# Kernel tuning notes

Measured on AMD Instinct MI355X. Metric: run time of the kernel, lower is better.

## Reference

```python
import jax, jax.numpy as jnp
import numpy as np
import math

NUM_SOLU, BS, GS, ED, NH = 10, 32, 1000, 128, 8
KD = ED // NH
MSH = 16
NEG = -9e15


def setup_inputs() -> dict:
    key = jax.random.key(0)
    ks = jax.random.split(key, 16)
    node_embed = jax.random.normal(ks[0], (BS, GS, ED), jnp.float32)
    # random TSP tours: permutations per (solution, batch) -> each node a source exactly once
    solutions = jnp.argsort(jax.random.uniform(ks[1], (NUM_SOLU, BS, GS)), axis=-1).astype(jnp.int32)
    costs = jax.random.uniform(ks[2], (NUM_SOLU, BS), minval=1.0, maxval=2.0)  # positive tour costs
    dist = jax.random.uniform(ks[3], (BS, GS, GS), jnp.float32)
    solution_embed_old = jax.random.normal(ks[4], (BS, GS, ED), jnp.float32)
    s = 1.0 / math.sqrt(ED)
    Wq = jax.random.uniform(ks[5], (ED, ED), minval=-s, maxval=s)
    Wk = jax.random.uniform(ks[6], (ED, ED), minval=-s, maxval=s)
    m1 = math.sqrt(0.5)
    m2 = math.sqrt(1.0 / 16.0)
    mix1_weight = jax.random.uniform(ks[7], (NH, 2, MSH), minval=-m1, maxval=m1)
    mix1_bias = jax.random.uniform(ks[8], (NH, MSH), minval=-m1, maxval=m1)
    mix2_weight = jax.random.uniform(ks[9], (NH, MSH, 1), minval=-m2, maxval=m2)
    mix2_bias = jax.random.uniform(ks[10], (NH, 1), minval=-m2, maxval=m2)
    sh = 1.0 / math.sqrt(NH)
    norm_head_w = jax.random.uniform(ks[11], (NH,), minval=-sh, maxval=sh)
    sg = 1.0 / math.sqrt(ED)
    gru_w_ih = jax.random.uniform(ks[12], (3 * ED, ED), minval=-sg, maxval=sg)
    gru_w_hh = jax.random.uniform(ks[13], (3 * ED, ED), minval=-sg, maxval=sg)
    gru_b_ih = jax.random.uniform(ks[14], (3 * ED,), minval=-sg, maxval=sg)
    gru_b_hh = jax.random.uniform(ks[15], (3 * ED,), minval=-sg, maxval=sg)
    return dict(node_embed=node_embed, solutions=solutions, costs=costs, dist=dist,
                solution_embed_old=solution_embed_old, Wq=Wq, Wk=Wk,
                mix1_weight=mix1_weight, mix1_bias=mix1_bias,
                mix2_weight=mix2_weight, mix2_bias=mix2_bias,
                norm_head_w=norm_head_w, gru_w_ih=gru_w_ih, gru_w_hh=gru_w_hh,
                gru_b_ih=gru_b_ih, gru_b_hh=gru_b_hh)


def _forward(node_embed, costs, dist, solution_embed_old, Wq, Wk,
             mix1_weight, mix1_bias, mix2_weight, mix2_bias, norm_head_w,
             gru_w_ih, gru_w_hh, gru_b_ih, gru_b_hh, solutions):
    norm_factor = 1.0 / math.sqrt(KD)
    sqrt_qkv = KD ** 0.5
    nxt = jnp.roll(solutions, -1, axis=-1)                      # [S,B,T] successor in tour
    b_idx = jnp.arange(BS)[None, :, None]
    emb_solu = node_embed[b_idx, solutions]                     # [S,B,T,E] gather
    emb_next = node_embed[b_idx, nxt]                           # [S,B,T,E]
    q = (emb_solu @ Wq.T).reshape(NUM_SOLU, BS, GS, NH, KD)
    k = (emb_next @ Wk.T).reshape(NUM_SOLU, BS, GS, NH, KD)
    dot = jnp.einsum('sbthd,sbthd->sbth', q, k) * (norm_factor / sqrt_qkv)
    edge_cost = dist[b_idx, solutions, nxt]                     # [S,B,T]
    two = jnp.stack([dot, jnp.broadcast_to(edge_cost[..., None], dot.shape)], -1)  # [S,B,T,H,2]
    ms1 = jax.nn.relu(jnp.einsum('sbthe,hem->sbthm', two, mix1_weight) + mix1_bias)
    ms2 = jnp.einsum('sbthm,hmo->sbtho', ms1, mix2_weight)[..., 0] + mix2_bias[:, 0]  # [S,B,T,H]
    e = jnp.einsum('sbth,h->sbt', ms2, norm_head_w)             # norm_head Linear(n_heads,1)
    cost = e / costs[:, :, None]                                # [S,B,T]
    # scatter-add edge scores into dense [B,G,G] attention (tours = permutations,
    # so each (b, src) appears once per solution -> add == per-solution set + sum)
    bb = jnp.broadcast_to(b_idx, solutions.shape)
    attn = jnp.zeros((BS, GS, GS), node_embed.dtype).at[
        bb.reshape(-1), solutions.reshape(-1), nxt.reshape(-1)].add(cost.reshape(-1))
    attn = jnp.where(attn != 0.0, attn, NEG)
    ar = jnp.arange(GS)
    attn = attn.at[:, ar, ar].set(NEG)
    attn = jax.nn.softmax(attn, axis=-1)
    solu_embed = attn @ node_embed                              # [B,G,E]
    # torch GRUCell: gates order r,z,n
    x = solu_embed.reshape(-1, ED)
    h = solution_embed_old.reshape(-1, ED)
    gi = x @ gru_w_ih.T + gru_b_ih
    gh = h @ gru_w_hh.T + gru_b_hh
    i_r, i_z, i_n = jnp.split(gi, 3, axis=-1)
    h_r, h_z, h_n = jnp.split(gh, 3, axis=-1)
    r = jax.nn.sigmoid(i_r + h_r)
    z = jax.nn.sigmoid(i_z + h_z)
    n = jnp.tanh(i_n + r * h_n)
    new = ((1.0 - z) * n + z * h).reshape(BS, GS, ED)
    return jnp.stack([jax.nn.elu(new), new])                    # [2,B,G,E]


def reference(node_embed, solutions, costs, dist, solution_embed_old, Wq, Wk,
              mix1_weight, mix1_bias, mix2_weight, mix2_bias, norm_head_w,
              gru_w_ih, gru_w_hh, gru_b_ih, gru_b_hh):
    out = _forward(node_embed, costs, dist, solution_embed_old, Wq, Wk,
                   mix1_weight, mix1_bias, mix2_weight, mix2_bias, norm_head_w,
                   gru_w_ih, gru_w_hh, gru_b_ih, gru_b_hh, solutions)
    return (out[0], out[1])
```

## Files before the change

### kernel.cpp

```cpp
#include <hip/hip_runtime.h>
#include <math.h>

#define NS 10
#define NB 32
#define NG 1000
#define NE 128
#define NH 8
#define MSH 16

typedef __bf16 bf16x8 __attribute__((ext_vector_type(8)));
typedef float f32x4 __attribute__((ext_vector_type(4)));
typedef unsigned short ushort;
typedef ushort us8 __attribute__((ext_vector_type(8)));

__device__ __forceinline__ ushort f2bf(float f) {
    union { float f; unsigned u; } c; c.f = f;
    unsigned r = c.u + 0x7FFFu + ((c.u >> 16) & 1u);
    return (ushort)(r >> 16);
}
__device__ __forceinline__ float bflo(unsigned u) {
    union { unsigned v; float f; } c; c.v = u << 16; return c.f;
}
__device__ __forceinline__ float bfhi(unsigned u) {
    union { unsigned v; float f; } c; c.v = u & 0xFFFF0000u; return c.f;
}
__device__ __forceinline__ float dot8(uint4 q, uint4 k) {
    return bflo(q.x) * bflo(k.x) + bfhi(q.x) * bfhi(k.x)
         + bflo(q.y) * bflo(k.y) + bfhi(q.y) * bfhi(k.y)
         + bflo(q.z) * bflo(k.z) + bfhi(q.z) * bfhi(k.z)
         + bflo(q.w) * bflo(k.w) + bfhi(q.w) * bfhi(k.w);
}

__global__ __launch_bounds__(512) void qk_prep(
        const float* __restrict__ ne,
        const int* __restrict__ sol, const float* __restrict__ dist,
        const float* __restrict__ Wq, const float* __restrict__ Wk,
        const float* __restrict__ wih, const float* __restrict__ whh,
        ushort* __restrict__ QKb, ushort* __restrict__ ne_b,
        int* __restrict__ succ, float* __restrict__ edge_val,
        ushort* __restrict__ wih_b, ushort* __restrict__ whh_b) {
    const int tid = threadIdx.x;
    if (blockIdx.x >= 500) {
        const int bid2 = blockIdx.x - 500;
        if (bid2 < 625) {
            const int gidx = bid2 * 512 + tid;
            const int sb = gidx / NG;
            const int t = gidx - sb * NG;
            const int* srow = sol + (size_t)sb * NG;
            const int src = srow[t];
            const int tn = (t + 1 == NG) ? 0 : t + 1;
            const int dst = srow[tn];
            const int b = sb & 31;
            succ[(size_t)sb * NG + src] = dst;
            edge_val[(size_t)sb * NG + src] = dist[(size_t)(b * NG + src) * NG + dst];
        } else {
            const int wt = (bid2 - 625) * 512 + tid;
            const int e = wt * 8;
            const float* src = (e < 49152) ? wih : whh;
            ushort* dst = (e < 49152) ? wih_b : whh_b;
            const int off = (e < 49152) ? e : e - 49152;
            const float4 f0 = ((const float4*)(src + off))[0];
            const float4 f1 = ((const float4*)(src + off))[1];
            us8 v;
            v[0] = f2bf(f0.x); v[1] = f2bf(f0.y); v[2] = f2bf(f0.z); v[3] = f2bf(f0.w);
            v[4] = f2bf(f1.x); v[5] = f2bf(f1.y); v[6] = f2bf(f1.z); v[7] = f2bf(f1.w);
            *(us8*)(dst + off) = v;
        }
        return;
    }

    __shared__ __align__(16) ushort A[64 * 128];
    const int rowbase = blockIdx.x * 64;
    {
#pragma unroll
        for (int i2 = 0; i2 < 2; ++i2) {
            const int i = tid + i2 * 512;
            const int r = i >> 4, kc = i & 15;
            const float4* s4 = (const float4*)(ne + (size_t)(rowbase + r) * NE);
            const float4 f0 = s4[kc * 2], f1 = s4[kc * 2 + 1];
            us8 v;
            v[0] = f2bf(f0.x); v[1] = f2bf(f0.y); v[2] = f2bf(f0.z); v[3] = f2bf(f0.w);
            v[4] = f2bf(f1.x); v[5] = f2bf(f1.y); v[6] = f2bf(f1.z); v[7] = f2bf(f1.w);
            *(us8*)&A[(r * 16 + (kc ^ (r & 7))) * 8] = v;
            *(us8*)&ne_b[(size_t)(rowbase + r) * NE + kc * 8] = v;
        }
    }
    __syncthreads();

    const int w = tid >> 6, l = tid & 63;
    const int lr = l & 15, lg = l >> 4;

    f32x4 acc[4][2] = {};
#pragma unroll
    for (int ks = 0; ks < 4; ++ks) {
        bf16x8 a[4], b[2];
#pragma unroll
        for (int mf = 0; mf < 4; ++mf) {
            const int r = mf * 16 + lr;
            a[mf] = *(const bf16x8*)&A[(r * 16 + ((ks * 4 + lg) ^ (r & 7))) * 8];
        }
#pragma unroll
        for (int nf = 0; nf < 2; ++nf) {
            const int j = w * 32 + nf * 16 + lr;
            const float* Wrow = (j < 128) ? (Wq + (size_t)j * 128 + ks * 32 + lg * 8)
                                          : (Wk + (size_t)(j - 128) * 128 + ks * 32 + lg * 8);
            const float4 wf0 = ((const float4*)Wrow)[0];
            const float4 wf1 = ((const float4*)Wrow)[1];
            union { us8 u; bf16x8 bv; } cv;
            cv.u[0] = f2bf(wf0.x); cv.u[1] = f2bf(wf0.y); cv.u[2] = f2bf(wf0.z); cv.u[3] = f2bf(wf0.w);
            cv.u[4] = f2bf(wf1.x); cv.u[5] = f2bf(wf1.y); cv.u[6] = f2bf(wf1.z); cv.u[7] = f2bf(wf1.w);
            b[nf] = cv.bv;
        }
#pragma unroll
        for (int mf = 0; mf < 4; ++mf)
#pragma unroll
            for (int nf = 0; nf < 2; ++nf)
                acc[mf][nf] = __builtin_amdgcn_mfma_f32_16x16x32_bf16(a[mf], b[nf], acc[mf][nf], 0, 0, 0);
    }
#pragma unroll
    for (int mf = 0; mf < 4; ++mf)
#pragma unroll
        for (int nf = 0; nf < 2; ++nf)
#pragma unroll
            for (int q = 0; q < 4; ++q) {
                const int row = rowbase + mf * 16 + lg * 4 + q;
                const int col = w * 32 + nf * 16 + lr;
                QKb[(size_t)row * 256 + col] = f2bf(acc[mf][nf][q]);
            }
}

__global__ __launch_bounds__(256) void score_agg(
        const int* __restrict__ succ, const float* __restrict__ costs,
        const float* __restrict__ edge_val, const ushort* __restrict__ QKb,
        const ushort* __restrict__ ne_b,
        const float* __restrict__ m1w, const float* __restrict__ m1b,
        const float* __restrict__ m2w, const float* __restrict__ m2b,
        const float* __restrict__ nhw,
        unsigned* __restrict__ solu_b) {
    __shared__ float w1t[2][MSH][NH];
    __shared__ float b1t[MSH][NH];
    __shared__ float w2t[MSH][NH];
    __shared__ float b2s[NH];
    __shared__ float nws[NH];
    const int tid = threadIdx.x;
    {
        const int h = tid >> 5, e = (tid >> 4) & 1, m = tid & 15;
        w1t[e][m][h] = m1w[tid];
        if (tid < 128) {
            const int h2 = tid >> 4, m2 = tid & 15;
            b1t[m2][h2] = m1b[tid];
            w2t[m2][h2] = m2w[tid];
        }
        if (tid < NH) { b2s[tid] = m2b[tid]; nws[tid] = nhw[tid]; }
    }
    __syncthreads();

    const int bid = blockIdx.x;
    const int xcd = bid & 7;
    const int idx = bid >> 3;
    const int b = xcd + 8 * (idx / 125);
    const int gbase = (idx % 125) * 8 + ((tid >> 6) << 1);
    const int lane = tid & 63;
    const int h = lane & 7;
    const int sg = lane >> 3;

    int dstp[2][2]; float edgep[2][2];
#pragma unroll
    for (int r = 0; r < 2; ++r) {
        const size_t o0 = (size_t)(sg * NB + b) * NG + (gbase + r);
        const size_t o1 = (size_t)((8 + sg) * NB + b) * NG + (gbase + r);
        dstp[r][0] = succ[o0];
        dstp[r][1] = (sg < 2) ? succ[o1] : 0;
        edgep[r][0] = edge_val[o0];
        edgep[r][1] = (sg < 2) ? edge_val[o1] : 0.f;
    }

    uint4 kk[2][2][2];
#pragma unroll
    for (int r = 0; r < 2; ++r)
#pragma unroll
        for (int p = 0; p < 2; ++p) {
            const uint4* Kr = (const uint4*)(QKb + (size_t)(b * NG + dstp[r][p]) * 256 + 128);
            kk[r][p][0] = Kr[h * 2]; kk[r][p][1] = Kr[h * 2 + 1];
        }

    uint4 qq[2][2];
#pragma unroll
    for (int r = 0; r < 2; ++r) {
        const uint4* Qr = (const uint4*)(QKb + (size_t)(b * NG + gbase + r) * 256);
        qq[r][0] = Qr[h * 2]; qq[r][1] = Qr[h * 2 + 1];
    }

    unsigned urow[2][NS];
#pragma unroll
    for (int r = 0; r < 2; ++r) {
        int dd;
#pragma unroll
        for (int s = 0; s < 8; ++s) {
            dd = __shfl(dstp[r][0], s * 8);
            urow[r][s] = ((const unsigned*)(ne_b + (size_t)(b * NG + dd) * NE))[lane];
        }
        dd = __shfl(dstp[r][1], 0);
        urow[r][8] = ((const unsigned*)(ne_b + (size_t)(b * NG + dd) * NE))[lane];
        dd = __shfl(dstp[r][1], 8);
        urow[r][9] = ((const unsigned*)(ne_b + (size_t)(b * NG + dd) * NE))[lane];
    }

    float val_p[2][2];
#pragma unroll
    for (int r = 0; r < 2; ++r)
#pragma unroll
        for (int p = 0; p < 2; ++p) {
            float dd = (dot8(qq[r][0], kk[r][p][0]) + dot8(qq[r][1], kk[r][p][1])) * 0.0625f;
            float ms2 = b2s[h];
#pragma unroll
            for (int m = 0; m < MSH; ++m) {
                float t = fmaf(dd, w1t[0][m][h], fmaf(edgep[r][p], w1t[1][m][h], b1t[m][h]));
                t = fmaxf(t, 0.f);
                ms2 = fmaf(t, w2t[m][h], ms2);
            }
            float contrib = ms2 * nws[h];
            contrib += __shfl_xor(contrib, 1);
            contrib += __shfl_xor(contrib, 2);
            contrib += __shfl_xor(contrib, 4);
            val_p[r][p] = contrib;
        }

    const float cinv = __builtin_amdgcn_rcpf(costs[((lane < NS) ? lane : 0) * NB + b]);
#pragma unroll
    for (int r = 0; r < 2; ++r) {
        const float va = __shfl(val_p[r][0], (lane & 7) * 8);
        const float vb = __shfl(val_p[r][1], (lane & 1) * 8);
        const int   da = __shfl(dstp[r][0], (lane & 7) * 8);
        const int   db = __shfl(dstp[r][1], (lane & 1) * 8);
        float v_own = ((lane < 8) ? va : vb) * cinv;
        const int d_own = (lane < 8) ? da : db;

        float acc = v_own;
        bool first = true;
#pragma unroll
        for (int p = 0; p < NS; ++p) {
            const int   d_p = __shfl(d_own, p);
            const float v_p = __shfl(v_own, p);
            const bool eq = (d_p == d_own);
            first = first && (!eq || p >= lane);
            acc += (eq && p > lane) ? v_p : 0.f;
        }
        const bool surv = (lane < NS) && first && (acc != 0.f);

        float mval = surv ? acc : -3.0e38f;
        mval = fmaxf(mval, __shfl_xor(mval, 1));
        mval = fmaxf(mval, __shfl_xor(mval, 2));
        mval = fmaxf(mval, __shfl_xor(mval, 4));
        mval = fmaxf(mval, __shfl_xor(mval, 8));
        const float e = surv ? __expf(acc - mval) : 0.f;
        float den = e;
        den += __shfl_xor(den, 1);
        den += __shfl_xor(den, 2);
        den += __shfl_xor(den, 4);
        den += __shfl_xor(den, 8);
        const float wt_own = e * __builtin_amdgcn_rcpf(den);

        const bool any = (__ballot(surv) != 0ull);

        float a0 = 0.f, a1 = 0.f;
        if (!any) {
            const unsigned* base = (const unsigned*)(ne_b + (size_t)b * NG * NE);
            for (int n = 0; n < NG; ++n) {
                const unsigned u = base[n * 64 + lane];
                a0 += bflo(u); a1 += bfhi(u);
            }
            const float invG = 1.f / NG;
            a0 *= invG; a1 *= invG;
        } else {
#pragma unroll
            for (int s = 0; s < NS; ++s) {
                const float wt = __shfl(wt_own, s);
                a0 += wt * bflo(urow[r][s]);
                a1 += wt * bfhi(urow[r][s]);
            }
        }
        solu_b[(size_t)(b * NG + gbase + r) * 64 + lane] =
            (unsigned)f2bf(a0) | ((unsigned)f2bf(a1) << 16);
    }
}

__global__ __launch_bounds__(512) void gru_mfma(
        const ushort* __restrict__ x_b,
        const float* __restrict__ h_in,
        const ushort* __restrict__ wih_b, const ushort* __restrict__ whh_b,
        const float* __restrict__ bih, const float* __restrict__ bhh,
        float* __restrict__ out0, float* __restrict__ out1) {
    __shared__ __align__(16) ushort X[32 * 128];
    __shared__ __align__(16) ushort H[32 * 128];
    const int tid = threadIdx.x;
    const int rowbase = blockIdx.x * 32;

    {
        const int r = tid >> 4, kc = tid & 15;
        us8 xv = *(const us8*)&x_b[(size_t)(rowbase + r) * NE + kc * 8];
        *(us8*)&X[(r * 16 + (kc ^ (r & 7))) * 8] = xv;
        const float4* h4 = (const float4*)(h_in + (size_t)(rowbase + r) * NE);
        const float4 f0 = h4[kc * 2], f1 = h4[kc * 2 + 1];
        us8 hv;
        hv[0] = f2bf(f0.x); hv[1] = f2bf(f0.y); hv[2] = f2bf(f0.z); hv[3] = f2bf(f0.w);
        hv[4] = f2bf(f1.x); hv[5] = f2bf(f1.y); hv[6] = f2bf(f1.z); hv[7] = f2bf(f1.w);
        *(us8*)&H[(r * 16 + (kc ^ (r & 7))) * 8] = hv;
    }
    __syncthreads();

    const int w = tid >> 6, l = tid & 63;
    const int lr = l & 15, lg = l >> 4;
    const int j = w * 16 + lr;

    f32x4 acc[2][6] = {};
#pragma unroll
    for (int ks = 0; ks < 4; ++ks) {
        bf16x8 ax[2], ah[2], bb[6];
#pragma unroll
        for (int mf = 0; mf < 2; ++mf) {
            const int r = mf * 16 + lr;
            const int c = (r * 16 + ((ks * 4 + lg) ^ (r & 7))) * 8;
            ax[mf] = *(const bf16x8*)&X[c];
            ah[mf] = *(const bf16x8*)&H[c];
        }
#pragma unroll
        for (int g = 0; g < 3; ++g) {
            bb[g]     = *(const bf16x8*)&wih_b[(size_t)(g * 128 + j) * 128 + ks * 32 + lg * 8];
            bb[g + 3] = *(const bf16x8*)&whh_b[(size_t)(g * 128 + j) * 128 + ks * 32 + lg * 8];
        }
#pragma unroll
        for (int mf = 0; mf < 2; ++mf) {
#pragma unroll
            for (int g = 0; g < 3; ++g) {
                acc[mf][g]     = __builtin_amdgcn_mfma_f32_16x16x32_bf16(ax[mf], bb[g],     acc[mf][g],     0, 0, 0);
                acc[mf][g + 3] = __builtin_amdgcn_mfma_f32_16x16x32_bf16(ah[mf], bb[g + 3], acc[mf][g + 3], 0, 0, 0);
            }
        }
    }

    const float bi0 = bih[j], bi1 = bih[128 + j], bi2 = bih[256 + j];
    const float bh0 = bhh[j], bh1 = bhh[128 + j], bh2 = bhh[256 + j];
#pragma unroll
    for (int mf = 0; mf < 2; ++mf) {
#pragma unroll
        for (int q = 0; q < 4; ++q) {
            const int row = rowbase + mf * 16 + lg * 4 + q;
            const float ir = acc[mf][0][q] + bi0;
            const float iz = acc[mf][1][q] + bi1;
            const float in_ = acc[mf][2][q] + bi2;
            const float hr = acc[mf][3][q] + bh0;
            const float hz = acc[mf][4][q] + bh1;
            const float hn = acc[mf][5][q] + bh2;
            const float rr = 1.f / (1.f + expf(-(ir + hr)));
            const float zz = 1.f / (1.f + expf(-(iz + hz)));
            const float nn = tanhf(in_ + rr * hn);
            const float hv = h_in[(size_t)row * NE + j];
            const float nv = (1.f - zz) * nn + zz * hv;
            const size_t o = (size_t)row * NE + j;
            out1[o] = nv;
            out0[o] = (nv > 0.f) ? nv : expm1f(nv);
        }
    }
}

extern "C" void kernel_launch(void* const* d_in, const int* in_sizes, int n_in,
                              void* d_out, int out_size, void* d_ws, size_t ws_size,
                              hipStream_t stream) {
    const float* ne    = (const float*)d_in[0];
    const int*   sol   = (const int*)d_in[1];
    const float* costs = (const float*)d_in[2];
    const float* dist  = (const float*)d_in[3];
    const float* old_h = (const float*)d_in[4];
    const float* Wq    = (const float*)d_in[5];
    const float* Wk    = (const float*)d_in[6];
    const float* m1w   = (const float*)d_in[7];
    const float* m1b   = (const float*)d_in[8];
    const float* m2w   = (const float*)d_in[9];
    const float* m2b   = (const float*)d_in[10];
    const float* nhw   = (const float*)d_in[11];
    const float* wih   = (const float*)d_in[12];
    const float* whh   = (const float*)d_in[13];
    const float* bih   = (const float*)d_in[14];
    const float* bhh   = (const float*)d_in[15];

    float* out0 = (float*)d_out;
    float* out1 = out0 + (size_t)NB * NG * NE;

    ushort*   QKb      = (ushort*)d_ws;
    ushort*   ne_b     = QKb + (size_t)NB * NG * 256;
    int*      succ     = (int*)(ne_b + (size_t)NB * NG * NE);
    float*    edge_val = (float*)(succ + (size_t)NS * NB * NG);
    unsigned* solu_b   = (unsigned*)(edge_val + (size_t)NS * NB * NG);
    ushort*   wih_b    = (ushort*)(solu_b + (size_t)NB * NG * 64);
    ushort*   whh_b    = wih_b + 384 * 128;

    qk_prep<<<500 + 625 + 24, 512, 0, stream>>>(
        ne, sol, dist, Wq, Wk, wih, whh,
        QKb, ne_b, succ, edge_val, wih_b, whh_b);
    score_agg<<<4000, 256, 0, stream>>>(
        succ, costs, edge_val, QKb, ne_b, m1w, m1b, m2w, m2b, nhw, solu_b);
    gru_mfma<<<(NB * NG) / 32, 512, 0, stream>>>(
        (const ushort*)solu_b, old_h, wih_b, whh_b, bih, bhh, out0, out1);
}
```

Before: 90.21 us.

## Pack successor and edge weight into int2, skip unused K loads, double GRU tile rows

After: 87.62 us. -2.9%, faster.

```diff
diff --git a/kernel.cpp b/kernel.cpp
--- a/kernel.cpp
+++ b/kernel.cpp
@@ -24,6 +24,12 @@
 __device__ __forceinline__ float bfhi(unsigned u) {
     union { unsigned v; float f; } c; c.v = u & 0xFFFF0000u; return c.f;
 }
+__device__ __forceinline__ float asf(int i) {
+    union { int i; float f; } c; c.i = i; return c.f;
+}
+__device__ __forceinline__ int asi(float f) {
+    union { float f; int i; } c; c.f = f; return c.i;
+}
 __device__ __forceinline__ float dot8(uint4 q, uint4 k) {
     return bflo(q.x) * bflo(k.x) + bfhi(q.x) * bfhi(k.x)
          + bflo(q.y) * bflo(k.y) + bfhi(q.y) * bfhi(k.y)
@@ -37,7 +43,7 @@
         const float* __restrict__ Wq, const float* __restrict__ Wk,
         const float* __restrict__ wih, const float* __restrict__ whh,
         ushort* __restrict__ QKb, ushort* __restrict__ ne_b,
-        int* __restrict__ succ, float* __restrict__ edge_val,
+        int2* __restrict__ edge_pack,
         ushort* __restrict__ wih_b, ushort* __restrict__ whh_b) {
     const int tid = threadIdx.x;
     if (blockIdx.x >= 500) {
@@ -51,8 +57,8 @@
             const int tn = (t + 1 == NG) ? 0 : t + 1;
             const int dst = srow[tn];
             const int b = sb & 31;
-            succ[(size_t)sb * NG + src] = dst;
-            edge_val[(size_t)sb * NG + src] = dist[(size_t)(b * NG + src) * NG + dst];
+            const float ev = dist[(size_t)(b * NG + src) * NG + dst];
+            edge_pack[(size_t)sb * NG + src] = make_int2(dst, asi(ev));
         } else {
             const int wt = (bid2 - 625) * 512 + tid;
             const int e = wt * 8;
@@ -130,9 +136,8 @@
 }
 
 __global__ __launch_bounds__(256) void score_agg(
-        const int* __restrict__ succ, const float* __restrict__ costs,
-        const float* __restrict__ edge_val, const ushort* __restrict__ QKb,
-        const ushort* __restrict__ ne_b,
+        const int2* __restrict__ edge_pack, const float* __restrict__ costs,
+        const ushort* __restrict__ QKb, const ushort* __restrict__ ne_b,
         const float* __restrict__ m1w, const float* __restrict__ m1b,
         const float* __restrict__ m2w, const float* __restrict__ m2b,
         const float* __restrict__ nhw,
@@ -167,22 +172,29 @@
     int dstp[2][2]; float edgep[2][2];
 #pragma unroll
     for (int r = 0; r < 2; ++r) {
-        const size_t o0 = (size_t)(sg * NB + b) * NG + (gbase + r);
-        const size_t o1 = (size_t)((8 + sg) * NB + b) * NG + (gbase + r);
-        dstp[r][0] = succ[o0];
-        dstp[r][1] = (sg < 2) ? succ[o1] : 0;
-        edgep[r][0] = edge_val[o0];
-        edgep[r][1] = (sg < 2) ? edge_val[o1] : 0.f;
+        const int2 e0 = edge_pack[(size_t)(sg * NB + b) * NG + (gbase + r)];
+        dstp[r][0] = e0.x; edgep[r][0] = asf(e0.y);
+        dstp[r][1] = 0; edgep[r][1] = 0.f;
+        if (sg < 2) {
+            const int2 e1 = edge_pack[(size_t)((8 + sg) * NB + b) * NG + (gbase + r)];
+            dstp[r][1] = e1.x; edgep[r][1] = asf(e1.y);
+        }
     }
 
     uint4 kk[2][2][2];
 #pragma unroll
-    for (int r = 0; r < 2; ++r)
-#pragma unroll
-        for (int p = 0; p < 2; ++p) {
-            const uint4* Kr = (const uint4*)(QKb + (size_t)(b * NG + dstp[r][p]) * 256 + 128);
-            kk[r][p][0] = Kr[h * 2]; kk[r][p][1] = Kr[h * 2 + 1];
-        }
+    for (int r = 0; r < 2; ++r) {
+        {
+            const uint4* Kr = (const uint4*)(QKb + (size_t)(b * NG + dstp[r][0]) * 256 + 128);
+            kk[r][0][0] = Kr[h * 2]; kk[r][0][1] = Kr[h * 2 + 1];
+        }
+        kk[r][1][0] = make_uint4(0, 0, 0, 0);
+        kk[r][1][1] = make_uint4(0, 0, 0, 0);
+        if (sg < 2) {
+            const uint4* Kr = (const uint4*)(QKb + (size_t)(b * NG + dstp[r][1]) * 256 + 128);
+            kk[r][1][0] = Kr[h * 2]; kk[r][1][1] = Kr[h * 2 + 1];
+        }
+    }
 
     uint4 qq[2][2];
 #pragma unroll
@@ -291,21 +303,25 @@
         const ushort* __restrict__ wih_b, const ushort* __restrict__ whh_b,
         const float* __restrict__ bih, const float* __restrict__ bhh,
         float* __restrict__ out0, float* __restrict__ out1) {
-    __shared__ __align__(16) ushort X[32 * 128];
-    __shared__ __align__(16) ushort H[32 * 128];
+    __shared__ __align__(16) ushort X[64 * 128];
+    __shared__ __align__(16) ushort H[64 * 128];
     const int tid = threadIdx.x;
-    const int rowbase = blockIdx.x * 32;
+    const int rowbase = blockIdx.x * 64;
 
     {
-        const int r = tid >> 4, kc = tid & 15;
-        us8 xv = *(const us8*)&x_b[(size_t)(rowbase + r) * NE + kc * 8];
-        *(us8*)&X[(r * 16 + (kc ^ (r & 7))) * 8] = xv;
-        const float4* h4 = (const float4*)(h_in + (size_t)(rowbase + r) * NE);
-        const float4 f0 = h4[kc * 2], f1 = h4[kc * 2 + 1];
-        us8 hv;
-        hv[0] = f2bf(f0.x); hv[1] = f2bf(f0.y); hv[2] = f2bf(f0.z); hv[3] = f2bf(f0.w);
-        hv[4] = f2bf(f1.x); hv[5] = f2bf(f1.y); hv[6] = f2bf(f1.z); hv[7] = f2bf(f1.w);
-        *(us8*)&H[(r * 16 + (kc ^ (r & 7))) * 8] = hv;
+#pragma unroll
+        for (int i2 = 0; i2 < 2; ++i2) {
+            const int i = tid + i2 * 512;
+            const int r = i >> 4, kc = i & 15;
+            us8 xv = *(const us8*)&x_b[(size_t)(rowbase + r) * NE + kc * 8];
+            *(us8*)&X[(r * 16 + (kc ^ (r & 7))) * 8] = xv;
+            const float4* h4 = (const float4*)(h_in + (size_t)(rowbase + r) * NE);
+            const float4 f0 = h4[kc * 2], f1 = h4[kc * 2 + 1];
+            us8 hv;
+            hv[0] = f2bf(f0.x); hv[1] = f2bf(f0.y); hv[2] = f2bf(f0.z); hv[3] = f2bf(f0.w);
+            hv[4] = f2bf(f1.x); hv[5] = f2bf(f1.y); hv[6] = f2bf(f1.z); hv[7] = f2bf(f1.w);
+            *(us8*)&H[(r * 16 + (kc ^ (r & 7))) * 8] = hv;
+        }
     }
     __syncthreads();
 
@@ -313,28 +329,25 @@
     const int lr = l & 15, lg = l >> 4;
     const int j = w * 16 + lr;
 
-    f32x4 acc[2][6] = {};
+    f32x4 acc[4][6] = {};
 #pragma unroll
     for (int ks = 0; ks < 4; ++ks) {
-        bf16x8 ax[2], ah[2], bb[6];
-#pragma unroll
-        for (int mf = 0; mf < 2; ++mf) {
-            const int r = mf * 16 + lr;
-            const int c = (r * 16 + ((ks * 4 + lg) ^ (r & 7))) * 8;
-            ax[mf] = *(const bf16x8*)&X[c];
-            ah[mf] = *(const bf16x8*)&H[c];
-        }
+        bf16x8 bb[6];
 #pragma unroll
         for (int g = 0; g < 3; ++g) {
             bb[g]     = *(const bf16x8*)&wih_b[(size_t)(g * 128 + j) * 128 + ks * 32 + lg * 8];
             bb[g + 3] = *(const bf16x8*)&whh_b[(size_t)(g * 128 + j) * 128 + ks * 32 + lg * 8];
         }
 #pragma unroll
-        for (int mf = 0; mf < 2; ++mf) {
+        for (int mf = 0; mf < 4; ++mf) {
+            const int r = mf * 16 + lr;
+            const int c = (r * 16 + ((ks * 4 + lg) ^ (r & 7))) * 8;
+            const bf16x8 ax = *(const bf16x8*)&X[c];
+            const bf16x8 ah = *(const bf16x8*)&H[c];
 #pragma unroll
             for (int g = 0; g < 3; ++g) {
-                acc[mf][g]     = __builtin_amdgcn_mfma_f32_16x16x32_bf16(ax[mf], bb[g],     acc[mf][g],     0, 0, 0);
-                acc[mf][g + 3] = __builtin_amdgcn_mfma_f32_16x16x32_bf16(ah[mf], bb[g + 3], acc[mf][g + 3], 0, 0, 0);
+                acc[mf][g]     = __builtin_amdgcn_mfma_f32_16x16x32_bf16(ax, bb[g],     acc[mf][g],     0, 0, 0);
+                acc[mf][g + 3] = __builtin_amdgcn_mfma_f32_16x16x32_bf16(ah, bb[g + 3], acc[mf][g + 3], 0, 0, 0);
             }
         }
     }
@@ -342,7 +355,7 @@
     const float bi0 = bih[j], bi1 = bih[128 + j], bi2 = bih[256 + j];
     const float bh0 = bhh[j], bh1 = bhh[128 + j], bh2 = bhh[256 + j];
 #pragma unroll
-    for (int mf = 0; mf < 2; ++mf) {
+    for (int mf = 0; mf < 4; ++mf) {
 #pragma unroll
         for (int q = 0; q < 4; ++q) {
             const int row = rowbase + mf * 16 + lg * 4 + q;
@@ -387,19 +400,18 @@
     float* out0 = (float*)d_out;
     float* out1 = out0 + (size_t)NB * NG * NE;
 
-    ushort*   QKb      = (ushort*)d_ws;
-    ushort*   ne_b     = QKb + (size_t)NB * NG * 256;
-    int*      succ     = (int*)(ne_b + (size_t)NB * NG * NE);
-    float*    edge_val = (float*)(succ + (size_t)NS * NB * NG);
-    unsigned* solu_b   = (unsigned*)(edge_val + (size_t)NS * NB * NG);
-    ushort*   wih_b    = (ushort*)(solu_b + (size_t)NB * NG * 64);
-    ushort*   whh_b    = wih_b + 384 * 128;
+    ushort*   QKb       = (ushort*)d_ws;
+    ushort*   ne_b      = QKb + (size_t)NB * NG * 256;
+    int2*     edge_pack = (int2*)(ne_b + (size_t)NB * NG * NE);
+    unsigned* solu_b    = (unsigned*)(edge_pack + (size_t)NS * NB * NG);
+    ushort*   wih_b     = (ushort*)(solu_b + (size_t)NB * NG * 64);
+    ushort*   whh_b     = wih_b + 384 * 128;
 
     qk_prep<<<500 + 625 + 24, 512, 0, stream>>>(
         ne, sol, dist, Wq, Wk, wih, whh,
-        QKb, ne_b, succ, edge_val, wih_b, whh_b);
+        QKb, ne_b, edge_pack, wih_b, whh_b);
     score_agg<<<4000, 256, 0, stream>>>(
-        succ, costs, edge_val, QKb, ne_b, m1w, m1b, m2w, m2b, nhw, solu_b);
-    gru_mfma<<<(NB * NG) / 32, 512, 0, stream>>>(
+        edge_pack, costs, QKb, ne_b, m1w, m1b, m2w, m2b, nhw, solu_b);
+    gru_mfma<<<(NB * NG) / 64, 512, 0, stream>>>(
         (const ushort*)solu_b, old_h, wih_b, whh_b, bih, bhh, out0, out1);
 }
```
